# Kernel tuning notes

Measured on AMD Instinct MI355X. Metric: run time of the kernel, lower is better.

The kernel has to match this reference:

```python
import jax, jax.numpy as jnp
import numpy as np

B, S, D = 2, 2048, 2048
H, KVH, HD = 8, 1, 256
N_REP = H // KVH
WIN = 1024
THETA = 10000.0
SCALE = 1.0 / (HD ** 0.5)


def setup_inputs() -> dict:
    key = jax.random.key(0)
    k1, k2, k3, k4, k5 = jax.random.split(key, 5)
    hidden_states = jax.random.normal(k1, (B, S, D), dtype=jnp.float32)
    neg = jnp.finfo(jnp.float32).min
    causal = jnp.where(jnp.tril(jnp.ones((S, S), jnp.float32)) == 1.0, 0.0, neg)
    attention_mask = jnp.broadcast_to(causal[None, None], (B, 1, S, S)).copy()
    position_ids = jnp.broadcast_to(jnp.arange(S, dtype=jnp.int32)[None, :], (B, S)).copy()
    std = 0.02
    Wq = std * jax.random.normal(k2, (H * HD, D), dtype=jnp.float32)
    Wk = std * jax.random.normal(k3, (KVH * HD, D), dtype=jnp.float32)
    Wv = std * jax.random.normal(k4, (KVH * HD, D), dtype=jnp.float32)
    Wo = std * jax.random.normal(k5, (D, H * HD), dtype=jnp.float32)
    return {"hidden_states": hidden_states, "attention_mask": attention_mask,
            "position_ids": position_ids, "Wq": Wq, "Wk": Wk, "Wv": Wv, "Wo": Wo}


def _rotate_half(x):
    x1, x2 = x[..., : HD // 2], x[..., HD // 2:]
    return jnp.concatenate([-x2, x1], axis=-1)


def _rope(position_ids):
    inv_freq = 1.0 / (THETA ** (jnp.arange(0, HD, 2, dtype=jnp.float32) / HD))  # [HD/2]
    freqs = position_ids.astype(jnp.float32)[:, :, None] * inv_freq  # [b,s,HD/2]
    emb = jnp.concatenate([freqs, freqs], axis=-1)  # [b,s,HD]
    # unsqueeze at head dim -> [b,1,s,HD]
    return jnp.cos(emb)[:, None], jnp.sin(emb)[:, None]


def reference(hidden_states, attention_mask, position_ids, Wq, Wk, Wv, Wo):
    b, s, _ = hidden_states.shape
    q = (hidden_states @ Wq.T).reshape(b, s, H, HD).transpose(0, 2, 1, 3)    # [b,H,s,hd]
    k = (hidden_states @ Wk.T).reshape(b, s, KVH, HD).transpose(0, 2, 1, 3)  # [b,KVH,s,hd]
    v = (hidden_states @ Wv.T).reshape(b, s, KVH, HD).transpose(0, 2, 1, 3)

    cos, sin = _rope(position_ids)
    q = q * cos + _rotate_half(q) * sin
    k = k * cos + _rotate_half(k) * sin

    neg = jnp.finfo(attention_mask.dtype).min
    ones = jnp.ones_like(attention_mask)
    sliding = jnp.triu(ones, -(WIN - 1)) * jnp.tril(ones, WIN - 1)
    mask = jnp.where(sliding == 1.0, attention_mask, neg)  # [b,1,s,s]

    # GQA without materializing repeated KV: group query heads by kv head
    qg = q.reshape(b, KVH, N_REP, s, HD)
    scores = jnp.einsum('bgrqd,bgkd->bgrqk', qg, k) * SCALE
    scores = scores + mask[:, :, None]  # broadcast over rep dim
    probs = jax.nn.softmax(scores, axis=-1)
    out = jnp.einsum('bgrqk,bgkd->bgrqd', probs, v)  # [b,KVH,rep,s,hd]
    out = out.reshape(b, H, s, HD).transpose(0, 2, 1, 3).reshape(b, s, H * HD)
    return out @ Wo.T
```

## Files before the change

### kernel.cpp

```cpp
#include <hip/hip_runtime.h>
#include <stdint.h>

typedef __attribute__((ext_vector_type(8))) short bf16x8;
typedef __attribute__((ext_vector_type(4))) float f32x4;
typedef __attribute__((ext_vector_type(4))) unsigned short u16x4;

#define LOG2E 1.44269504088896340736f
#define SCALE 0.0625f

__device__ __forceinline__ unsigned short f32_bf16(float f) {
  unsigned int u = __float_as_uint(f);
  u += 0x7fffu + ((u >> 16) & 1u);
  return (unsigned short)(u >> 16);
}
__device__ __forceinline__ float bf16_f32(unsigned short h) {
  return __uint_as_float(((unsigned int)h) << 16);
}

__device__ __forceinline__ void gload16(const unsigned short* g, unsigned short* l) {
  __builtin_amdgcn_global_load_lds((const __attribute__((address_space(1))) void*)g,
                                   (__attribute__((address_space(3))) void*)l, 16, 0, 0);
}

__global__ void cast_kernel(const float* __restrict__ in, unsigned short* __restrict__ out, int n4) {
  int i = blockIdx.x * blockDim.x + threadIdx.x;
  if (i >= n4) return;
  const float4 v = ((const float4*)in)[i];
  u16x4 o;
  o[0] = f32_bf16(v.x); o[1] = f32_bf16(v.y); o[2] = f32_bf16(v.z); o[3] = f32_bf16(v.w);
  ((u16x4*)out)[i] = o;
}

template<int OUTF32>
__global__ __launch_bounds__(256) void gemm_nt(const unsigned short* __restrict__ A,
                                               const unsigned short* __restrict__ B,
                                               void* __restrict__ Cp,
                                               int M, int N, int K) {
  __shared__ unsigned short As[128 * 32];
  __shared__ unsigned short Bs[128 * 32];
  const int t = threadIdx.x;
  const int lane = t & 63;
  const int wave = t >> 6;
  const int wr = (wave >> 1) * 64;
  const int wc = (wave & 1) * 64;
  const long m0 = (long)blockIdx.y * 128;
  const long n0 = (long)blockIdx.x * 128;
  const int l15 = lane & 15, lg = lane >> 4;

  f32x4 acc[4][4];
#pragma unroll
  for (int m = 0; m < 4; ++m)
#pragma unroll
    for (int n = 0; n < 4; ++n) acc[m][n] = (f32x4){0.f, 0.f, 0.f, 0.f};

  const int srow = t >> 2;
  const int scol = (t & 3) * 8;
  const unsigned short* Ag = A + (m0 + srow) * (long)K + scol;
  const unsigned short* Bg = B + (n0 + srow) * (long)K + scol;

  for (int k0 = 0; k0 < K; k0 += 32) {
    gload16(Ag + k0, &As[t * 8]);
    gload16(Ag + (long)64 * K + k0, &As[2048 + t * 8]);
    gload16(Bg + k0, &Bs[t * 8]);
    gload16(Bg + (long)64 * K + k0, &Bs[2048 + t * 8]);
    __syncthreads();
    bf16x8 af[4], bfr[4];
#pragma unroll
    for (int m = 0; m < 4; ++m) af[m] = *(const bf16x8*)&As[(wr + m * 16 + l15) * 32 + lg * 8];
#pragma unroll
    for (int n = 0; n < 4; ++n) bfr[n] = *(const bf16x8*)&Bs[(wc + n * 16 + l15) * 32 + lg * 8];
#pragma unroll
    for (int m = 0; m < 4; ++m)
#pragma unroll
      for (int n = 0; n < 4; ++n)
        acc[m][n] = __builtin_amdgcn_mfma_f32_16x16x32_bf16(af[m], bfr[n], acc[m][n], 0, 0, 0);
    __syncthreads();
  }

#pragma unroll
  for (int m = 0; m < 4; ++m)
#pragma unroll
    for (int n = 0; n < 4; ++n)
#pragma unroll
      for (int r = 0; r < 4; ++r) {
        long row = m0 + wr + m * 16 + lg * 4 + r;
        long col = n0 + wc + n * 16 + l15;
        if (OUTF32)
          ((float*)Cp)[row * N + col] = acc[m][n][r];
        else
          ((unsigned short*)Cp)[row * N + col] = f32_bf16(acc[m][n][r]);
      }
}

__global__ void rope_table(const int* __restrict__ pos, float* __restrict__ ctab,
                           float* __restrict__ stab) {
  int i = blockIdx.x * blockDim.x + threadIdx.x;
  int d = i & 127;
  int s = (i >> 7) & 2047;
  int b = i >> 18;
  float p = (float)pos[b * 2048 + s];
  float f = p * exp2f(-(float)d * 0.10381025296523f);
  float sn, c;
  sincosf(f, &sn, &c);
  ctab[i] = c;
  stab[i] = sn;
}

__global__ void rope_apply(unsigned short* __restrict__ qkv, const float* __restrict__ ctab,
                           const float* __restrict__ stab) {
  int i = blockIdx.x * blockDim.x + threadIdx.x;
  int g = i & 15;
  int hh = (i >> 4) % 9;
  int sb_ = (i >> 4) / 9;
  int s = sb_ & 2047;
  int b = sb_ >> 11;
  size_t base = (size_t)(b * 2048 + s) * 2560 + (hh == 8 ? 2048 : hh * 256) + g * 8;
  const float* ct = ctab + ((size_t)(b * 2048 + s) << 7) + g * 8;
  const float* st = stab + ((size_t)(b * 2048 + s) << 7) + g * 8;
  bf16x8 lo = *(const bf16x8*)(qkv + base);
  bf16x8 hi = *(const bf16x8*)(qkv + base + 128);
  bf16x8 lo2, hi2;
#pragma unroll
  for (int e = 0; e < 8; ++e) {
    float c = ct[e], sn = st[e];
    float x1 = bf16_f32((unsigned short)lo[e]);
    float x2 = bf16_f32((unsigned short)hi[e]);
    lo2[e] = (short)f32_bf16(x1 * c - x2 * sn);
    hi2[e] = (short)f32_bf16(x2 * c + x1 * sn);
  }
  *(bf16x8*)(qkv + base) = lo2;
  *(bf16x8*)(qkv + base + 128) = hi2;
}

__global__ __launch_bounds__(256) void transpose_v(const unsigned short* __restrict__ qkv,
                                                   unsigned short* __restrict__ vt) {
  __shared__ unsigned short tile[64][68];
  const int t = threadIdx.x;
  const int s0 = blockIdx.x * 64, d0 = blockIdx.y * 64, b = blockIdx.z;
  const int r = t >> 4, c4 = (t & 15) * 4;
#pragma unroll
  for (int j = 0; j < 4; ++j) {
    int row = r + j * 16;
    const unsigned short* src = qkv + (size_t)(b * 2048 + s0 + row) * 2560 + 2304 + d0 + c4;
#pragma unroll
    for (int e = 0; e < 4; ++e) tile[row][c4 + e] = src[e];
  }
  __syncthreads();
#pragma unroll
  for (int j = 0; j < 4; ++j) {
    int drow = r + j * 16;
    u16x4 o;
#pragma unroll
    for (int e = 0; e < 4; ++e) o[e] = tile[c4 + e][drow];
    *(u16x4*)(vt + (size_t)(b * 256 + d0 + drow) * 2048 + s0 + c4) = o;
  }
}

__global__ __launch_bounds__(256) void attn2(const unsigned short* __restrict__ qkv,
                                             const unsigned short* __restrict__ vt,
                                             unsigned short* __restrict__ O) {
  __shared__ __align__(16) unsigned short Ks[2][32 * 256];
  __shared__ __align__(16) unsigned short Vs[2][256 * 32];
  const int t = threadIdx.x, lane = t & 63, wave = t >> 6;
  const int l15 = lane & 15, lg = lane >> 4;
  const int qb = blockIdx.x, h = blockIdx.y, b = blockIdx.z;
  const int q0 = qb * 64;
  const int qg = q0 + wave * 16 + l15;

  bf16x8 qf[8];
  {
    const unsigned short* qp = qkv + (size_t)(b * 2048 + qg) * 2560 + h * 256 + lg * 8;
#pragma unroll
    for (int c = 0; c < 8; ++c) qf[c] = *(const bf16x8*)(qp + c * 32);
  }

  size_t kgb[4], vgb[4];
  int klo[4], vlo[4];
#pragma unroll
  for (int p = 0; p < 4; ++p) {
    int i = p * 256 + t;
    int kr = i >> 5, kb = (i & 31) << 4;
    int ksrc = kb ^ ((kr & 7) << 4);
    kgb[p] = (size_t)(b * 2048 + kr) * 2560 + 2048 + (ksrc >> 1);
    klo[p] = i * 8;
    int vr = i >> 2, vb = (i & 3) << 4;
    int vsrc = vb ^ ((vr & 3) << 4);
    vgb[p] = (size_t)(b * 256 + vr) * 2048 + (vsrc >> 1);
    vlo[p] = i * 8;
  }

  f32x4 oacc[16];
#pragma unroll
  for (int dt = 0; dt < 16; ++dt) oacc[dt] = (f32x4){0.f, 0.f, 0.f, 0.f};
  float mrun = -3e30f, lrun = 0.f;

  int ks0 = q0 - 1023;
  if (ks0 < 0) ks0 = 0;
  ks0 &= ~31;
  const int nst = (q0 + 64 - ks0) >> 5;

#pragma unroll
  for (int p = 0; p < 4; ++p) gload16(qkv + kgb[p] + (size_t)ks0 * 2560, &Ks[0][klo[p]]);
#pragma unroll
  for (int p = 0; p < 4; ++p) gload16(vt + vgb[p] + ks0, &Vs[0][vlo[p]]);
  __syncthreads();

  for (int si = 0; si < nst; ++si) {
    const int ks = ks0 + si * 32;
    const int cur = si & 1;
    if (si + 1 < nst) {
      const size_t ko = (size_t)(ks + 32) * 2560;
#pragma unroll
      for (int p = 0; p < 4; ++p) gload16(qkv + kgb[p] + ko, &Ks[cur ^ 1][klo[p]]);
#pragma unroll
      for (int p = 0; p < 4; ++p) gload16(vt + vgb[p] + (ks + 32), &Vs[cur ^ 1][vlo[p]]);
    }
    const unsigned short* Kc = Ks[cur];
    const unsigned short* Vc = Vs[cur];

    f32x4 sa = (f32x4){0.f, 0.f, 0.f, 0.f};
    f32x4 sb2 = (f32x4){0.f, 0.f, 0.f, 0.f};
    const int kswz = (l15 & 7) << 4;
#pragma unroll
    for (int c = 0; c < 8; ++c) {
      const int off = ((c * 64 + lg * 16) ^ kswz) >> 1;
      bf16x8 k0 = *(const bf16x8*)&Kc[l15 * 256 + off];
      bf16x8 k1 = *(const bf16x8*)&Kc[(16 + l15) * 256 + off];
      sa = __builtin_amdgcn_mfma_f32_16x16x32_bf16(k0, qf[c], sa, 0, 0, 0);
      sb2 = __builtin_amdgcn_mfma_f32_16x16x32_bf16(k1, qf[c], sb2, 0, 0, 0);
    }

    float pv[8];
    const int kb0 = ks + lg * 4, kb1 = kb0 + 16;
    const int lo_b = qg - 1024;
#pragma unroll
    for (int r = 0; r < 4; ++r) {
      int k0i = kb0 + r, k1i = kb1 + r;
      pv[r] = (k0i <= qg && k0i > lo_b) ? sa[r] * SCALE : -3e38f;
      pv[4 + r] = (k1i <= qg && k1i > lo_b) ? sb2[r] * SCALE : -3e38f;
    }
    float mx = fmaxf(fmaxf(fmaxf(pv[0], pv[1]), fmaxf(pv[2], pv[3])),
                     fmaxf(fmaxf(pv[4], pv[5]), fmaxf(pv[6], pv[7])));
    mx = fmaxf(mx, __shfl_xor(mx, 16));
    mx = fmaxf(mx, __shfl_xor(mx, 32));
    if (!__all(mx - mrun <= 8.0f)) {
      float mnew = fmaxf(mrun, mx);
      float al = exp2f((mrun - mnew) * LOG2E);
#pragma unroll
      for (int dt = 0; dt < 16; ++dt) oacc[dt] *= al;
      lrun *= al;
      mrun = mnew;
    }
    float ps = 0.f;
#pragma unroll
    for (int j = 0; j < 8; ++j) {
      pv[j] = exp2f((pv[j] - mrun) * LOG2E);
      ps += pv[j];
    }
    ps += __shfl_xor(ps, 16);
    ps += __shfl_xor(ps, 32);
    lrun += ps;

    unsigned int w0 = ((unsigned int)f32_bf16(pv[1]) << 16) | f32_bf16(pv[0]);
    unsigned int w1 = ((unsigned int)f32_bf16(pv[3]) << 16) | f32_bf16(pv[2]);
    unsigned int w2 = ((unsigned int)f32_bf16(pv[5]) << 16) | f32_bf16(pv[4]);
    unsigned int w3 = ((unsigned int)f32_bf16(pv[7]) << 16) | f32_bf16(pv[6]);
    const int srcA = l15 + ((lg & 1) << 5);
    const int srcB = srcA + 16;
    unsigned int a0 = __shfl((int)w0, srcA), a1 = __shfl((int)w1, srcA);
    unsigned int a2 = __shfl((int)w2, srcA), a3 = __shfl((int)w3, srcA);
    unsigned int b0 = __shfl((int)w0, srcB), b1 = __shfl((int)w1, srcB);
    unsigned int b2 = __shfl((int)w2, srcB), b3 = __shfl((int)w3, srcB);
    union { unsigned int u[4]; bf16x8 v; } pu;
    const bool hi2 = (lg >> 1) != 0;
    pu.u[0] = hi2 ? a2 : a0;
    pu.u[1] = hi2 ? a3 : a1;
    pu.u[2] = hi2 ? b2 : b0;
    pu.u[3] = hi2 ? b3 : b1;

    const int vswz = (lg * 16) ^ ((l15 & 3) << 4);
#pragma unroll
    for (int dt = 0; dt < 16; ++dt) {
      bf16x8 vf = *(const bf16x8*)&Vc[(dt * 16 + l15) * 32 + (vswz >> 1)];
      oacc[dt] = __builtin_amdgcn_mfma_f32_16x16x32_bf16(vf, pu.v, oacc[dt], 0, 0, 0);
    }
    __syncthreads();
  }

  float inv = 1.0f / lrun;
  unsigned short* op = O + (size_t)(b * 2048 + qg) * 2048 + h * 256 + lg * 4;
#pragma unroll
  for (int dt = 0; dt < 16; ++dt) {
    u16x4 o4;
#pragma unroll
    for (int r = 0; r < 4; ++r) o4[r] = f32_bf16(oacc[dt][r] * inv);
    *(u16x4*)(op + dt * 16) = o4;
  }
}

extern "C" void kernel_launch(void* const* d_in, const int* in_sizes, int n_in,
                              void* d_out, int out_size, void* d_ws, size_t ws_size,
                              hipStream_t stream) {
  const float* hidden = (const float*)d_in[0];
  const int* pos_ids = (const int*)d_in[2];
  const float* Wq = (const float*)d_in[3];
  const float* Wk = (const float*)d_in[4];
  const float* Wv = (const float*)d_in[5];
  const float* Wo = (const float*)d_in[6];
  float* out = (float*)d_out;
  char* ws = (char*)d_ws;

  unsigned short* qkv_bf = (unsigned short*)(ws);
  unsigned short* hid_bf = (unsigned short*)(ws + 20971520);
  unsigned short* w_bf   = (unsigned short*)(ws + 37748736);
  unsigned short* vtbuf  = (unsigned short*)(ws + 48234496);
  float*          ctab   = (float*)(ws + 50331648);
  float*          stab   = (float*)(ws + 52428800);
  unsigned short* attno  = hid_bf;

  cast_kernel<<<8192, 256, 0, stream>>>(hidden, hid_bf, 2097152);
  cast_kernel<<<4096, 256, 0, stream>>>(Wq, w_bf, 1048576);
  cast_kernel<<<512, 256, 0, stream>>>(Wk, w_bf + 4194304, 131072);
  cast_kernel<<<512, 256, 0, stream>>>(Wv, w_bf + 4718592, 131072);

  gemm_nt<0><<<dim3(20, 32), 256, 0, stream>>>(hid_bf, w_bf, qkv_bf, 4096, 2560, 2048);

  cast_kernel<<<4096, 256, 0, stream>>>(Wo, w_bf, 1048576);

  rope_table<<<2048, 256, 0, stream>>>(pos_ids, ctab, stab);
  rope_apply<<<2304, 256, 0, stream>>>(qkv_bf, ctab, stab);

  transpose_v<<<dim3(32, 4, 2), 256, 0, stream>>>(qkv_bf, vtbuf);

  attn2<<<dim3(32, 8, 2), 256, 0, stream>>>(qkv_bf, vtbuf, attno);

  gemm_nt<1><<<dim3(16, 32), 256, 0, stream>>>(attno, w_bf, out, 4096, 2048, 2048);
}
```

Baseline: 360.4 us.

## Double-buffer GEMM LDS, remap workgroups, retune V swizzle and P shuffles

The GEMM now double-buffers its LDS tiles so the next K-slice loads while the current one runs through MFMA. It also remaps workgroup IDs so neighbouring tiles land on the same XCD for better L2 locality. Both kernels raise wave priority around MFMA blocks with s_setprio. The attention kernel changes the V-tile LDS swizzle to reduce bank conflicts and swaps eight indexed shuffles for four xor shuffles when rebuilding the P fragment. In exchange, GEMM LDS use doubles, which may lower occupancy.

```diff
diff --git a/kernel.cpp b/kernel.cpp
--- a/kernel.cpp
+++ b/kernel.cpp
@@ -36,16 +36,23 @@
                                                const unsigned short* __restrict__ B,
                                                void* __restrict__ Cp,
                                                int M, int N, int K) {
-  __shared__ unsigned short As[128 * 32];
-  __shared__ unsigned short Bs[128 * 32];
+  __shared__ unsigned short As[2][128 * 32];
+  __shared__ unsigned short Bs[2][128 * 32];
   const int t = threadIdx.x;
   const int lane = t & 63;
   const int wave = t >> 6;
   const int wr = (wave >> 1) * 64;
   const int wc = (wave & 1) * 64;
-  const long m0 = (long)blockIdx.y * 128;
-  const long n0 = (long)blockIdx.x * 128;
   const int l15 = lane & 15, lg = lane >> 4;
+
+  const int gx = gridDim.x, gy = gridDim.y;
+  int orig = blockIdx.y * gx + blockIdx.x;
+  int nwg = gx * gy;
+  int wg = orig;
+  if ((nwg & 7) == 0) wg = (orig & 7) * (nwg >> 3) + (orig >> 3);
+  const int bx = wg / gy, by = wg % gy;
+  const long m0 = (long)by * 128;
+  const long n0 = (long)bx * 128;
 
   f32x4 acc[4][4];
 #pragma unroll
@@ -58,23 +65,32 @@
   const unsigned short* Ag = A + (m0 + srow) * (long)K + scol;
   const unsigned short* Bg = B + (n0 + srow) * (long)K + scol;
 
+  auto stage = [&](int buf, int k0) {
+    gload16(Ag + k0, &As[buf][t * 8]);
+    gload16(Ag + (long)64 * K + k0, &As[buf][2048 + t * 8]);
+    gload16(Bg + k0, &Bs[buf][t * 8]);
+    gload16(Bg + (long)64 * K + k0, &Bs[buf][2048 + t * 8]);
+  };
+
+  stage(0, 0);
+  __syncthreads();
+  int cur = 0;
   for (int k0 = 0; k0 < K; k0 += 32) {
-    gload16(Ag + k0, &As[t * 8]);
-    gload16(Ag + (long)64 * K + k0, &As[2048 + t * 8]);
-    gload16(Bg + k0, &Bs[t * 8]);
-    gload16(Bg + (long)64 * K + k0, &Bs[2048 + t * 8]);
-    __syncthreads();
+    if (k0 + 32 < K) stage(cur ^ 1, k0 + 32);
     bf16x8 af[4], bfr[4];
 #pragma unroll
-    for (int m = 0; m < 4; ++m) af[m] = *(const bf16x8*)&As[(wr + m * 16 + l15) * 32 + lg * 8];
-#pragma unroll
-    for (int n = 0; n < 4; ++n) bfr[n] = *(const bf16x8*)&Bs[(wc + n * 16 + l15) * 32 + lg * 8];
+    for (int m = 0; m < 4; ++m) af[m] = *(const bf16x8*)&As[cur][(wr + m * 16 + l15) * 32 + lg * 8];
+#pragma unroll
+    for (int n = 0; n < 4; ++n) bfr[n] = *(const bf16x8*)&Bs[cur][(wc + n * 16 + l15) * 32 + lg * 8];
+    __builtin_amdgcn_s_setprio(1);
 #pragma unroll
     for (int m = 0; m < 4; ++m)
 #pragma unroll
       for (int n = 0; n < 4; ++n)
         acc[m][n] = __builtin_amdgcn_mfma_f32_16x16x32_bf16(af[m], bfr[n], acc[m][n], 0, 0, 0);
+    __builtin_amdgcn_s_setprio(0);
     __syncthreads();
+    cur ^= 1;
   }
 
 #pragma unroll
@@ -184,7 +200,7 @@
     kgb[p] = (size_t)(b * 2048 + kr) * 2560 + 2048 + (ksrc >> 1);
     klo[p] = i * 8;
     int vr = i >> 2, vb = (i & 3) << 4;
-    int vsrc = vb ^ ((vr & 3) << 4);
+    int vsrc = vb ^ (((vr >> 1) & 3) << 4);
     vgb[p] = (size_t)(b * 256 + vr) * 2048 + (vsrc >> 1);
     vlo[p] = i * 8;
   }
@@ -221,6 +237,7 @@
     f32x4 sa = (f32x4){0.f, 0.f, 0.f, 0.f};
     f32x4 sb2 = (f32x4){0.f, 0.f, 0.f, 0.f};
     const int kswz = (l15 & 7) << 4;
+    __builtin_amdgcn_s_setprio(1);
 #pragma unroll
     for (int c = 0; c < 8; ++c) {
       const int off = ((c * 64 + lg * 16) ^ kswz) >> 1;
@@ -229,6 +246,7 @@
       sa = __builtin_amdgcn_mfma_f32_16x16x32_bf16(k0, qf[c], sa, 0, 0, 0);
       sb2 = __builtin_amdgcn_mfma_f32_16x16x32_bf16(k1, qf[c], sb2, 0, 0, 0);
     }
+    __builtin_amdgcn_s_setprio(0);
 
     float pv[8];
     const int kb0 = ks + lg * 4, kb1 = kb0 + 16;
@@ -265,25 +283,31 @@
     unsigned int w1 = ((unsigned int)f32_bf16(pv[3]) << 16) | f32_bf16(pv[2]);
     unsigned int w2 = ((unsigned int)f32_bf16(pv[5]) << 16) | f32_bf16(pv[4]);
     unsigned int w3 = ((unsigned int)f32_bf16(pv[7]) << 16) | f32_bf16(pv[6]);
-    const int srcA = l15 + ((lg & 1) << 5);
-    const int srcB = srcA + 16;
-    unsigned int a0 = __shfl((int)w0, srcA), a1 = __shfl((int)w1, srcA);
-    unsigned int a2 = __shfl((int)w2, srcA), a3 = __shfl((int)w3, srcA);
-    unsigned int b0 = __shfl((int)w0, srcB), b1 = __shfl((int)w1, srcB);
-    unsigned int b2 = __shfl((int)w2, srcB), b3 = __shfl((int)w3, srcB);
+    unsigned int sA0 = (lg < 2) ? w2 : w0;
+    unsigned int sA1 = (lg < 2) ? w3 : w1;
+    unsigned int rA0 = (unsigned int)__shfl_xor((int)sA0, 32);
+    unsigned int rA1 = (unsigned int)__shfl_xor((int)sA1, 32);
+    unsigned int own0 = (lg < 2) ? w0 : w2;
+    unsigned int own1 = (lg < 2) ? w1 : w3;
+    const bool sendOwn = ((lg ^ (lg >> 1)) & 1) != 0;
+    unsigned int sB0 = sendOwn ? own0 : rA0;
+    unsigned int sB1 = sendOwn ? own1 : rA1;
+    unsigned int rB0 = (unsigned int)__shfl_xor((int)sB0, 16);
+    unsigned int rB1 = (unsigned int)__shfl_xor((int)sB1, 16);
     union { unsigned int u[4]; bf16x8 v; } pu;
-    const bool hi2 = (lg >> 1) != 0;
-    pu.u[0] = hi2 ? a2 : a0;
-    pu.u[1] = hi2 ? a3 : a1;
-    pu.u[2] = hi2 ? b2 : b0;
-    pu.u[3] = hi2 ? b3 : b1;
-
-    const int vswz = (lg * 16) ^ ((l15 & 3) << 4);
+    pu.u[0] = (lg == 0) ? own0 : ((lg == 2) ? rA0 : rB0);
+    pu.u[1] = (lg == 0) ? own1 : ((lg == 2) ? rA1 : rB1);
+    pu.u[2] = (lg == 3) ? own0 : ((lg == 1) ? rA0 : rB0);
+    pu.u[3] = (lg == 3) ? own1 : ((lg == 1) ? rA1 : rB1);
+
+    const int vswz = (lg * 16) ^ (((l15 >> 1) & 3) << 4);
+    __builtin_amdgcn_s_setprio(1);
 #pragma unroll
     for (int dt = 0; dt < 16; ++dt) {
       bf16x8 vf = *(const bf16x8*)&Vc[(dt * 16 + l15) * 32 + (vswz >> 1)];
       oacc[dt] = __builtin_amdgcn_mfma_f32_16x16x32_bf16(vf, pu.v, oacc[dt], 0, 0, 0);
     }
+    __builtin_amdgcn_s_setprio(0);
     __syncthreads();
   }
 
```

Measured after the change: 338.9 us. 1.06x faster.
